# Kernel optimization log

Hardware: AMD Instinct MI355X
Metric: run time of the kernel (lower is better)

The kernel has to match this reference:

```python
import jax, jax.numpy as jnp
import numpy as np

IMC = 256
EPS = 1e-6
BN_EPS = 1e-5
GRID = (69.12, 79.36)      # (depth, width) in meters
OFF = (0.0, -39.68, 0.0)   # (xoff, yoff, zoff)
RES = 0.64
ZMIN, ZMAX = -3.0, 2.76
SCALES = [0.25, 0.125, 0.0625, 0.03125, 0.015625]


def make_corners():
    # replicates make_grid(): corner lattice in lidar coords, shape [nz, nx, ny, 3]
    nx = int(round(GRID[0] / RES)) + 1   # 109
    ny = int(round(GRID[1] / RES)) + 1   # 125
    nz = int(round((ZMAX - ZMIN) / RES)) + 1  # 10
    xc = RES * np.arange(nx) + OFF[0]
    yc = GRID[1] - RES * np.arange(ny) + OFF[1]
    zc = ZMAX - RES * np.arange(nz)
    xx, yy = np.meshgrid(xc, yc, indexing='ij')
    base = np.stack([xx, yy, np.full_like(xx, OFF[2])], axis=-1)  # [nx,ny,3]
    zoffs = np.stack([np.zeros(nz), np.zeros(nz), zc], axis=-1)   # [nz,3]
    corners = base[None] + zoffs[:, None, None, :]
    return jnp.asarray(corners, jnp.float32)


def grid_sample(img, grid):
    # img [B,C,H,W]; grid [B,P,N,2] xy in [-1,1]; bilinear, zero padding, align_corners=False
    B, C, H, W = img.shape
    x = (grid[..., 0] + 1.0) * (W * 0.5) - 0.5
    y = (grid[..., 1] + 1.0) * (H * 0.5) - 0.5
    x0f = jnp.floor(x); y0f = jnp.floor(y)
    wx = (x - x0f).reshape(B, 1, -1)
    wy = (y - y0f).reshape(B, 1, -1)
    x0 = x0f.astype(jnp.int32); y0 = y0f.astype(jnp.int32)
    flat = img.reshape(B, C, H * W)
    def g(xi, yi):
        ok = ((xi >= 0) & (xi < W) & (yi >= 0) & (yi < H)).reshape(B, 1, -1)
        idx = (jnp.clip(yi, 0, H - 1) * W + jnp.clip(xi, 0, W - 1)).reshape(B, 1, -1)
        return jnp.take_along_axis(flat, idx, axis=2) * ok
    v00 = g(x0, y0); v01 = g(x0 + 1, y0); v10 = g(x0, y0 + 1); v11 = g(x0 + 1, y0 + 1)
    out = (v00 * (1 - wx) + v01 * wx) * (1 - wy) + (v10 * (1 - wx) + v11 * wx) * wy
    return out.reshape(B, C, grid.shape[1], grid.shape[2])


def oft(feats, calib, corners, scale, w, b):
    B, C, Hf, Wf = feats.shape
    # perspective projection of grid corners into the image plane
    hom = jnp.einsum('bij,zdwj->bzdwi', calib[:, :, :3], corners) + calib[:, None, None, None, :, 3]
    xy = hom[..., :2] / hom[..., 2:3]                      # [B,nz,nx,ny,2]
    img_size = jnp.array([Wf, Hf], jnp.float32) / scale
    nc = jnp.clip(2.0 * xy / img_size - 1.0, -1.0, 1.0)
    mn = jnp.minimum(nc[:, :-1, :-1, :-1], nc[:, :-1, 1:, :-1])
    mx = jnp.maximum(nc[:, 1:, 1:, 1:], nc[:, 1:, :-1, 1:])
    bbox = jnp.concatenate([mn, mx], axis=-1)              # [B,Zc,Dc,Wc,4]
    _, Zc, Dc, Wc, _ = bbox.shape
    bbox = bbox.reshape(B, Zc, Dc * Wc, 4)
    area = ((bbox[..., 2] - bbox[..., 0]) * (bbox[..., 3] - bbox[..., 1])
            * (Hf * Wf * 0.25) + EPS)[:, None]             # [B,1,Zc,N]
    visible = (area > EPS).astype(feats.dtype)
    ii = jnp.cumsum(jnp.cumsum(feats, axis=-1), axis=-2)   # integral image
    tl = grid_sample(ii, jnp.stack([bbox[..., 0], bbox[..., 1]], -1))
    br = grid_sample(ii, jnp.stack([bbox[..., 2], bbox[..., 3]], -1))
    tr = grid_sample(ii, jnp.stack([bbox[..., 2], bbox[..., 1]], -1))
    bl = grid_sample(ii, jnp.stack([bbox[..., 0], bbox[..., 3]], -1))
    vox = (tl + br - tr - bl) / area * visible             # [B,C,Zc,N]
    vox = vox.transpose(0, 3, 1, 2).reshape(B * Dc * Wc, C * Zc)
    ortho = jax.nn.relu(vox @ w.T + b).reshape(B, Dc, Wc, -1)
    return ortho.transpose(0, 3, 2, 1)                     # [B,imc,Wc,Dc]


def attention(x, aw, ab):
    s = jax.nn.sigmoid(x.mean(axis=(2, 3)) @ aw.T + ab)
    return x * s[:, :, None, None]


def conv3x3(x, w, stride):
    return jax.lax.conv_general_dilated(x, w, (stride, stride), ((1, 1), (1, 1)),
                                        dimension_numbers=('NCHW', 'OIHW', 'NCHW'))


def bn(x, g, b, m, v):
    scale = g / jnp.sqrt(v + BN_EPS)
    return (x - m[None, :, None, None]) * scale[None, :, None, None] + b[None, :, None, None]


def make_calib(B):
    K = np.array([[560.0, 0.0, 640.0], [0.0, 560.0, 192.0], [0.0, 0.0, 1.0]])
    Rt = np.array([[0.0, -1.0, 0.0, 0.05],   # lidar(x fwd, y left, z up) -> cam(x right, y down, z fwd)
                   [0.0, 0.0, -1.0, -0.30],
                   [1.0, 0.0, 0.0, 0.27]])
    P = K @ Rt
    return jnp.asarray(np.tile(P[None], (B, 1, 1)), jnp.float32)


def setup_inputs() -> dict:
    key = jax.random.key(0)
    ks = jax.random.split(key, 16)
    B = 1
    shapes = [(B, IMC, 96, 320), (B, IMC, 48, 160), (B, IMC, 24, 80), (B, IMC, 12, 40), (B, IMC, 6, 20)]
    feats = [jax.random.normal(ks[i], s, jnp.float32) * 0.1 for i, s in enumerate(shapes)]
    HC = 9 * IMC  # height_channels = int((2.76-(-3))/0.64 * 256) = 2304
    inp = {
        'feats04': feats[0], 'feats08': feats[1], 'feats16': feats[2],
        'feats32': feats[3], 'feats64': feats[4],
        'calib': make_calib(B),
        'oft_w': jax.random.normal(ks[5], (5, IMC, HC), jnp.float32) * 0.02,
        'oft_b': jax.random.normal(ks[6], (5, IMC), jnp.float32) * 0.02,
        'att_w': jax.random.normal(ks[7], (IMC, IMC), jnp.float32) * 0.05,
        'att_b': jnp.zeros((IMC,), jnp.float32),
        'conv1_w': jax.random.normal(ks[8], (IMC, IMC * 5, 3, 3), jnp.float32) * 0.02,
        'bn1_g': 1.0 + 0.1 * jax.random.normal(ks[9], (IMC,), jnp.float32),
        'bn1_b': 0.05 * jax.random.normal(ks[10], (IMC,), jnp.float32),
        'bn1_m': 0.05 * jax.random.normal(ks[11], (IMC,), jnp.float32),
        'bn1_v': jax.random.uniform(ks[12], (IMC,), jnp.float32, 0.5, 1.5),
        'conv2_w': jax.random.normal(ks[13], (IMC, IMC, 3, 3), jnp.float32) * 0.02,
        'bn2_g': 1.0 + 0.1 * jax.random.normal(ks[14], (IMC,), jnp.float32),
        'bn2_b': jnp.zeros((IMC,), jnp.float32),
        'bn2_m': jnp.zeros((IMC,), jnp.float32),
        'bn2_v': jax.random.uniform(ks[15], (IMC,), jnp.float32, 0.5, 1.5),
    }
    return inp


def reference(feats04, feats08, feats16, feats32, feats64, calib,
              oft_w, oft_b, att_w, att_b,
              conv1_w, bn1_g, bn1_b, bn1_m, bn1_v,
              conv2_w, bn2_g, bn2_b, bn2_m, bn2_v):
    corners = make_corners()
    feats = [feats04, feats08, feats16, feats32, feats64]
    orthos = [attention(oft(f, calib, corners, s, oft_w[i], oft_b[i]), att_w, att_b)
              for i, (f, s) in enumerate(zip(feats, SCALES))]
    x = jnp.concatenate(orthos, axis=1)            # [B, 5*imc, 124, 108]
    x = jax.nn.relu(bn(conv3x3(x, conv1_w, 2), bn1_g, bn1_b, bn1_m, bn1_v))
    x = jax.nn.relu(bn(conv3x3(x, conv2_w, 1), bn2_g, bn2_b, bn2_m, bn2_v))
    return x                                       # [B, imc, 62, 54]
```

## Files before the change

kernel.cpp:

```cpp
#include <hip/hip_runtime.h>

typedef __attribute__((ext_vector_type(8))) short short8;
typedef __attribute__((ext_vector_type(4))) float float4v;
typedef __attribute__((ext_vector_type(4))) int int4v;
typedef __attribute__((ext_vector_type(4))) unsigned short ushort4v;

#define NBOX 13392
#define ZC 9
#define KOFT 2304
#define NPIX 3348
#define NBLK0 105
#define NBLKC 27
#define TILEK 4096
#define NBSTRIDE 294912
#define OFT_SPLIT 4

__device__ __forceinline__ unsigned short f2bf(float f) {
  union { float f; unsigned int i; } v; v.f = f;
  unsigned int r = v.i + 0x7FFFu + ((v.i >> 16) & 1u);
  return (unsigned short)(r >> 16);
}
__device__ __forceinline__ float bf2f(unsigned short u) {
  union { unsigned int i; float f; } v; v.i = ((unsigned int)u) << 16; return v.f;
}
__device__ __forceinline__ float i2f(int i) {
  union { int i; float f; } v; v.i = i; return v.f;
}

__device__ __forceinline__ const int* uniform_ptr(const int* p) {
  unsigned lo = (unsigned)(uintptr_t)p;
  unsigned hi = (unsigned)((uintptr_t)p >> 32);
  lo = (unsigned)__builtin_amdgcn_readfirstlane((int)lo);
  hi = (unsigned)__builtin_amdgcn_readfirstlane((int)hi);
  return (const int*)(((uintptr_t)hi << 32) | (uintptr_t)lo);
}

__device__ __forceinline__ void async16(const unsigned short* g, unsigned short* l) {
  __builtin_amdgcn_global_load_lds(
      (const __attribute__((address_space(1))) unsigned int*)g,
      (__attribute__((address_space(3))) unsigned int*)l, 16, 0, 0);
}

__global__ void k_alpha_beta(const float* __restrict__ oft_b,
                             const float* __restrict__ g1, const float* __restrict__ b1,
                             const float* __restrict__ m1, const float* __restrict__ v1,
                             const float* __restrict__ g2, const float* __restrict__ b2,
                             const float* __restrict__ m2, const float* __restrict__ v2,
                             float* __restrict__ ALPHA, float* __restrict__ BETA,
                             float* __restrict__ MEANS, unsigned short* __restrict__ ZPAGE) {
  int g = blockIdx.x, c = threadIdx.x;
  float al, be;
  if (g < 5) { al = 1.f; be = oft_b[g * 256 + c]; MEANS[g * 256 + c] = 0.f; }
  else {
    const float* gg = (g == 5) ? g1 : g2;
    const float* bb = (g == 5) ? b1 : b2;
    const float* mm = (g == 5) ? m1 : m2;
    const float* vv = (g == 5) ? v1 : v2;
    al = gg[c] / sqrtf(vv[c] + 1e-5f);
    be = bb[c] - mm[c] * al;
  }
  ALPHA[g * 256 + c] = al; BETA[g * 256 + c] = be;
  if (g == 0) ZPAGE[c] = 0;
}

__global__ void k_wpermT(const float* __restrict__ w, unsigned short* __restrict__ wp) {
  int idx = blockIdx.x * 256 + threadIdx.x;
  int sc = idx / 589824;
  int r  = idx % 589824;
  int j   = r & 7;
  int row = (r >> 3) & 127;
  int kc  = (r >> 10) & 3;
  int cs  = r >> 12;
  int cb  = cs / 72, s = cs % 72;
  int oc = cb * 128 + row;
  int k  = s * 32 + kc * 8 + j;
  int z = k >> 8, c = k & 255;
  wp[idx] = f2bf(w[((size_t)sc * 256 + oc) * 2304 + c * 9 + z]);
}

__global__ void k_wperm1T(const float* __restrict__ w, const float* __restrict__ satt,
                          unsigned short* __restrict__ wp) {
  int idx = blockIdx.x * 256 + threadIdx.x;
  int j   = idx & 7;
  int row = (idx >> 3) & 127;
  int kc  = (idx >> 10) & 3;
  int rest = idx >> 12;
  int s = rest % 40; rest /= 40;
  int r = rest % 9;  int cb = rest / 9;
  int oc = cb * 128 + row;
  int ic = s * 32 + kc * 8 + j;
  wp[idx] = f2bf(w[(size_t)oc * 11520 + ic * 9 + r] * satt[ic]);
}

__global__ void k_wperm2T(const float* __restrict__ w, unsigned short* __restrict__ wp) {
  int idx = blockIdx.x * 256 + threadIdx.x;
  int j   = idx & 7;
  int row = (idx >> 3) & 127;
  int kc  = (idx >> 10) & 3;
  int rest = idx >> 12;
  int s = rest % 8; rest /= 8;
  int r = rest % 9; int cb = rest / 9;
  int oc = cb * 128 + row;
  int ic = s * 32 + kc * 8 + j;
  wp[idx] = f2bf(w[(size_t)oc * 2304 + ic * 9 + r]);
}

__global__ void k_taps(const float* __restrict__ calib, int* __restrict__ taps,
                       int Hf, int Wf, float areaScale) {
  int idx = blockIdx.x * 256 + threadIdx.x;
  if (idx >= ZC * NBOX) return;
  int z = idx / NBOX, n = idx % NBOX;
  int d = n / 124, wj = n % 124;
  float P[12];
#pragma unroll
  for (int i = 0; i < 12; ++i) P[i] = calib[i];
  auto proj = [&](int k, int i, int j, float& nxo, float& nyo) {
    float X = 0.64f * (float)i;
    float Y = 39.68f - 0.64f * (float)j;
    float Z = 2.76f - 0.64f * (float)k;
    float hx = P[0] * X + P[1] * Y + P[2]  * Z + P[3];
    float hy = P[4] * X + P[5] * Y + P[6]  * Z + P[7];
    float hz = P[8] * X + P[9] * Y + P[10] * Z + P[11];
    float px = hx / hz, py = hy / hz;
    nxo = 2.f * px / 1280.f - 1.f; nxo = fminf(fmaxf(nxo, -1.f), 1.f);
    nyo = 2.f * py / 384.f  - 1.f; nyo = fminf(fmaxf(nyo, -1.f), 1.f);
  };
  float ax, ay, bx, by, cx, cy, dx, dy;
  proj(z,     d,     wj,     ax, ay);
  proj(z,     d + 1, wj,     bx, by);
  proj(z + 1, d + 1, wj + 1, cx, cy);
  proj(z + 1, d,     wj + 1, dx, dy);
  float x0 = fminf(ax, bx), y0 = fminf(ay, by);
  float x1 = fmaxf(cx, dx), y1 = fmaxf(cy, dy);
  float rawA = (x1 - x0) * (y1 - y0) * areaScale;
  int* ob = taps + (size_t)idx * 32;
  if (!(rawA > 0.f)) { ob[0] = 0; return; }
  float inv = 1.f / (rawA + 1e-6f);

  float u0 = (x0 + 1.f) * ((float)Wf * 0.5f) - 0.5f;
  float u1 = (x1 + 1.f) * ((float)Wf * 0.5f) - 0.5f;
  float fu0 = floorf(u0), fu1 = floorf(u1);
  int cx0 = (int)fu0, cx1 = (int)fu1;
  float wx0 = u0 - fu0, wx1 = u1 - fu1;
  int xs[4]; float xw[4];
  xs[0] = cx0; xs[1] = cx0 + 1; xs[2] = cx1; xs[3] = cx1 + 1;
  xw[0] = (1.f - wx0) * inv; xw[1] = wx0 * inv;
  xw[2] = -(1.f - wx1) * inv; xw[3] = -wx1 * inv;
  int dcx = cx1 - cx0;
  if (dcx == 0)      { xw[0] += xw[2]; xw[1] += xw[3]; xw[2] = 0.f; xw[3] = 0.f; }
  else if (dcx == 1) { xw[1] += xw[2]; xw[2] = xw[3]; xs[2] = xs[3]; xw[3] = 0.f; }
#pragma unroll
  for (int j = 0; j < 4; ++j) {
    if (xs[j] < 0 || xs[j] >= Wf) xw[j] = 0.f;
    xs[j] = min(max(xs[j], 0), Wf - 1);
  }
#define CSWX(a, b) { if (xw[a] == 0.f && xw[b] != 0.f) { \
    float tw = xw[a]; xw[a] = xw[b]; xw[b] = tw; \
    int ts = xs[a]; xs[a] = xs[b]; xs[b] = ts; } }
  CSWX(0, 1) CSWX(2, 3) CSWX(0, 2) CSWX(1, 3) CSWX(1, 2)
#undef CSWX
  int nx = (xw[0] != 0.f) + (xw[1] != 0.f) + (xw[2] != 0.f) + (xw[3] != 0.f);

  float v0 = (y0 + 1.f) * ((float)Hf * 0.5f) - 0.5f;
  float v1 = (y1 + 1.f) * ((float)Hf * 0.5f) - 0.5f;
  float fv0 = floorf(v0), fv1 = floorf(v1);
  int ry0 = (int)fv0, ry1 = (int)fv1;
  float wy0 = v0 - fv0, wy1 = v1 - fv1;
  int ys[4]; float yw[4];
  ys[0] = ry0; ys[1] = ry0 + 1; ys[2] = ry1; ys[3] = ry1 + 1;
  yw[0] = 1.f - wy0; yw[1] = wy0; yw[2] = -(1.f - wy1); yw[3] = -wy1;
  int dcy = ry1 - ry0;
  if (dcy == 0)      { yw[0] += yw[2]; yw[1] += yw[3]; yw[2] = 0.f; yw[3] = 0.f; }
  else if (dcy == 1) { yw[1] += yw[2]; yw[2] = yw[3]; ys[2] = ys[3]; yw[3] = 0.f; }
#pragma unroll
  for (int j = 0; j < 4; ++j) {
    if (ys[j] < 0 || ys[j] >= Hf) yw[j] = 0.f;
    ys[j] = min(max(ys[j], 0), Hf - 1);
  }
#define CSWY(a, b) { if (yw[a] == 0.f && yw[b] != 0.f) { \
    float tw = yw[a]; yw[a] = yw[b]; yw[b] = tw; \
    int ts = ys[a]; ys[a] = ys[b]; ys[b] = ts; } }
  CSWY(0, 1) CSWY(2, 3) CSWY(0, 2) CSWY(1, 3) CSWY(1, 2)
#undef CSWY
  int ny = (yw[0] != 0.f) + (yw[1] != 0.f) + (yw[2] != 0.f) + (yw[3] != 0.f);

  if (nx == 0 || ny == 0) { ob[0] = 0; return; }

  int off[16]; float w[16];
#pragma unroll
  for (int r = 0; r < 4; ++r)
#pragma unroll
    for (int c = 0; c < 4; ++c) {
      off[r * 4 + c] = (ys[r] * Wf + xs[c]) * 1024;
      w[r * 4 + c] = yw[r] * xw[c];
    }
  off[0] |= (nx << 25) | (ny << 28);
  int4v* obv = (int4v*)ob;
#pragma unroll
  for (int i = 0; i < 4; ++i)
    obv[i] = (int4v){off[4 * i], off[4 * i + 1], off[4 * i + 2], off[4 * i + 3]};
  float4v* wb = (float4v*)obv;
#pragma unroll
  for (int i = 0; i < 4; ++i)
    wb[4 + i] = (float4v){w[4 * i], w[4 * i + 1], w[4 * i + 2], w[4 * i + 3]};
}

__global__ void k_transpose_all(const float* __restrict__ f0, const float* __restrict__ f1,
                                const float* __restrict__ f2, const float* __restrict__ f3,
                                const float* __restrict__ f4, float* __restrict__ II) {
  int b = blockIdx.x;
  int sc, cx;
  if (b < 480)      { sc = 0; cx = b; }
  else if (b < 600) { sc = 1; cx = b - 480; }
  else if (b < 630) { sc = 2; cx = b - 600; }
  else if (b < 638) { sc = 3; cx = b - 630; }
  else              { sc = 4; cx = b - 638; }
  const int Ss[5] = {30720, 7680, 1920, 480, 120};
  const size_t IIof[5] = {0, 7864320, 9830400, 10321920, 10444800};
  const float* srcs[5] = {f0, f1, f2, f3, f4};
  int S = Ss[sc];
  const float* src = srcs[sc];
  float* dst = II + IIof[sc];
  __shared__ float tile[64][65];
  int t = threadIdx.x;
  int wave = t >> 6, lane = t & 63;
  int s0 = cx * 64, c0 = blockIdx.y * 64;
#pragma unroll
  for (int i = 0; i < 16; ++i) {
    int c_l = wave * 16 + i;
    if (s0 + lane < S) tile[c_l][lane] = src[(size_t)(c0 + c_l) * S + s0 + lane];
  }
  __syncthreads();
#pragma unroll
  for (int i = 0; i < 16; ++i) {
    int s_l = wave * 16 + i;
    if (s0 + s_l < S) dst[(size_t)(s0 + s_l) * 256 + c0 + lane] = tile[lane][s_l];
  }
}

__global__ void k_cumw_all(float* __restrict__ II) {
  int b = blockIdx.x;
  int sc, h;
  if (b < 96)       { sc = 0; h = b; }
  else if (b < 144) { sc = 1; h = b - 96; }
  else if (b < 168) { sc = 2; h = b - 144; }
  else if (b < 180) { sc = 3; h = b - 168; }
  else              { sc = 4; h = b - 180; }
  const int Wfs[5] = {320, 160, 80, 40, 20};
  const size_t IIof[5] = {0, 7864320, 9830400, 10321920, 10444800};
  int Wf = Wfs[sc];
  float* p = II + IIof[sc] + (size_t)h * Wf * 256 + threadIdx.x;
  float acc = 0.f;
#pragma unroll 4
  for (int w = 0; w < Wf; ++w) { acc += p[(size_t)w * 256]; p[(size_t)w * 256] = acc; }
}

__global__ void k_cumh_all(float* __restrict__ II) {
  int b = blockIdx.x;
  int sc, w;
  if (b < 320)      { sc = 0; w = b; }
  else if (b < 480) { sc = 1; w = b - 320; }
  else if (b < 560) { sc = 2; w = b - 480; }
  else if (b < 600) { sc = 3; w = b - 560; }
  else              { sc = 4; w = b - 600; }
  const int Wfs[5] = {320, 160, 80, 40, 20};
  const int Hfs[5] = {96, 48, 24, 12, 6};
  const size_t IIof[5] = {0, 7864320, 9830400, 10321920, 10444800};
  int Hf = Hfs[sc];
  size_t stride = (size_t)Wfs[sc] * 256;
  float* p = II + IIof[sc] + (size_t)w * 256 + threadIdx.x;
  float acc = 0.f;
#pragma unroll 4
  for (int h = 0; h < Hf; ++h) { acc += p[h * stride]; p[h * stride] = acc; }
}

__global__ __launch_bounds__(512) void k_sample(const float* __restrict__ ii,
                                                const int* __restrict__ taps,
                                                unsigned short* __restrict__ voxT) {
  __shared__ unsigned short st[3][8][66][4];
  int t = threadIdx.x;
  int wave = t >> 6, lane = t & 63;
  int n = blockIdx.x * 8 + wave;
  int zg = blockIdx.y * 3;
  const char* iib = (const char*)ii + (lane << 4);
#pragma unroll
  for (int dz = 0; dz < 3; ++dz) {
    int z = zg + dz;
    const int* tb = uniform_ptr(taps + (size_t)(z * NBOX + n) * 32);
    int o_[16];
#pragma unroll
    for (int i = 0; i < 16; ++i) o_[i] = tb[i];
    unsigned h = (unsigned)o_[0];
    int nx = (h >> 25) & 7;
    int ny = (h >> 28) & 7;
    o_[0] = (int)(h & 0x01FFFFFFu);
    ushort4v o;
    if (ny == 0) {
      o[0] = 0; o[1] = 0; o[2] = 0; o[3] = 0;
    } else {
      float w_[16];
#pragma unroll
      for (int i = 0; i < 16; ++i) w_[i] = i2f(tb[16 + i]);
      float4v a0 = {0.f, 0.f, 0.f, 0.f}, a1 = a0;
#define TAP(i, acc) { float4v t_ = *(const float4v*)(iib + (size_t)(unsigned)o_[i]); acc += t_ * w_[i]; }
      TAP(0, a0)
      if (nx > 1) TAP(1, a1)
      if (nx > 2) TAP(2, a0)
      if (nx > 3) TAP(3, a1)
      if (ny > 1) {
        TAP(4, a0)
        if (nx > 1) TAP(5, a1)
        if (nx > 2) TAP(6, a0)
        if (nx > 3) TAP(7, a1)
      }
      if (ny > 2) {
        TAP(8, a0)
        if (nx > 1) TAP(9, a1)
        if (nx > 2) TAP(10, a0)
        if (nx > 3) TAP(11, a1)
      }
      if (ny > 3) {
        TAP(12, a0)
        if (nx > 1) TAP(13, a1)
        if (nx > 2) TAP(14, a0)
        if (nx > 3) TAP(15, a1)
      }
#undef TAP
      float4v acc = a0 + a1;
#pragma unroll
      for (int j = 0; j < 4; ++j) o[j] = f2bf(acc[j]);
    }
    *(ushort4v*)&st[dz][wave][lane][0] = o;
  }
  __syncthreads();
  int nb = (blockIdx.x * 8) >> 7;
  int r0 = (blockIdx.x * 8) & 127;
  unsigned short* outb = voxT + (size_t)nb * NBSTRIDE + (size_t)r0 * 32;
  int lane32 = t & 31;
  int row = lane32 >> 2, kc = lane32 & 3;
#pragma unroll
  for (int p = 0; p < 2; ++p) {
    int q = p * 16 + (t >> 5);
    if (q < 24) {
      int zq = q >> 3;
      int si = q & 7;
      short8 v = *(const short8*)&st[zq][row][si * 8 + kc * 2][0];
      *(short8*)(outb + (size_t)(zg + zq) * 32768 + (size_t)si * 4096
                 + (size_t)(row * 32 + kc * 8)) = v;
    }
  }
}

__global__ __launch_bounds__(256) void k_gemmT(
    const unsigned short* __restrict__ AT, const unsigned short* __restrict__ BT,
    float* __restrict__ part) {
  __shared__ unsigned short lsA[4096];
  __shared__ unsigned short lsB[4096];
  int t = threadIdx.x;
  int lane = t & 63, wave = t >> 6;
  int l15 = lane & 15, quad = lane >> 4;
  int nb = blockIdx.x, cb = blockIdx.y, ks = blockIdx.z;
  int wrow = (wave >> 1) * 64, wcol = (wave & 1) * 64;

  const unsigned short* ga = AT + (size_t)nb * NBSTRIDE + (size_t)ks * 18 * TILEK + t * 8;
  const unsigned short* gb = BT + (size_t)cb * NBSTRIDE + (size_t)ks * 18 * TILEK + t * 8;
  unsigned short* ldA = lsA + t * 8;
  unsigned short* ldB = lsB + t * 8;

  float4v acc[4][4];
#pragma unroll
  for (int mi = 0; mi < 4; ++mi)
#pragma unroll
    for (int ni = 0; ni < 4; ++ni) acc[mi][ni] = (float4v){0.f, 0.f, 0.f, 0.f};

  for (int s = 0; s < 18; ++s) {
    async16(ga, ldA);
    async16(ga + 2048, ldA + 2048);
    async16(gb, ldB);
    async16(gb + 2048, ldB + 2048);
    ga += TILEK; gb += TILEK;
    __syncthreads();
    short8 af[4], bf[4];
    const short8* pA = (const short8*)lsA;
    const short8* pB = (const short8*)lsB;
#pragma unroll
    for (int mi = 0; mi < 4; ++mi) af[mi] = pA[(wrow + mi * 16 + l15) * 4 + quad];
#pragma unroll
    for (int ni = 0; ni < 4; ++ni) bf[ni] = pB[quad * 128 + wcol + ni * 16 + l15];
#pragma unroll
    for (int mi = 0; mi < 4; ++mi)
#pragma unroll
      for (int ni = 0; ni < 4; ++ni)
        acc[mi][ni] = __builtin_amdgcn_mfma_f32_16x16x32_bf16(af[mi], bf[ni], acc[mi][ni], 0, 0, 0);
    __syncthreads();
  }

#pragma unroll
  for (int mi = 0; mi < 4; ++mi) {
    int nb0 = nb * 128 + wrow + mi * 16 + quad * 4;
#pragma unroll
    for (int j = 0; j < 4; ++j) {
      int nn = nb0 + j;
      if (nn < NBOX) {
#pragma unroll
        for (int ni = 0; ni < 4; ++ni) {
          int oc = cb * 128 + wcol + ni * 16 + l15;
          part[((size_t)ks * NBOX + nn) * 256 + oc] = acc[mi][ni][j];
        }
      }
    }
  }
}

__global__ void k_redoft(const float* __restrict__ part, const float* __restrict__ beta,
                         unsigned short* __restrict__ xbuf, int choff) {
  int n = blockIdx.x, oc = threadIdx.x;
  float v = part[(size_t)n * 256 + oc]
          + part[((size_t)NBOX + n) * 256 + oc]
          + part[((size_t)2 * NBOX + n) * 256 + oc]
          + part[((size_t)3 * NBOX + n) * 256 + oc];
  v += beta[oc];
  v = v > 0.f ? v : 0.f;
  xbuf[(size_t)n * 1280 + choff + oc] = f2bf(v);
}

template <int MODE>
__global__ __launch_bounds__(256) void k_gemmS(
    const unsigned short* __restrict__ A, const unsigned short* __restrict__ BT,
    float* __restrict__ part, const unsigned short* __restrict__ zpage) {
  constexpr int KIC   = (MODE == 1) ? 1280 : 256;
  constexpr int STEPS = KIC / 32;
  __shared__ unsigned short lsA[4096];
  __shared__ unsigned short lsB[4096];
  int t = threadIdx.x;
  int lane = t & 63, wave = t >> 6;
  int l15 = lane & 15, quad = lane >> 4;
  int n0 = blockIdx.x * 128, oc0 = blockIdx.y * 128;
  int r = blockIdx.z;
  int wrow = (wave >> 1) * 64, wcol = (wave & 1) * 64;
  int srow = t & 127, skc = t >> 7;

  int p = n0 + srow;
  int oy = p / 54, ox = p - oy * 54;
  int ky = r / 3, kx = r - ky * 3;
  bool valid; int sp;
  if (MODE == 1) {
    int ih = 2 * oy + ky - 1, iw = 2 * ox + kx - 1;
    valid = (p < NPIX) && ((unsigned)ih < 124u) && ((unsigned)iw < 108u);
    sp = iw * 124 + ih;
  } else {
    int ih = oy + ky - 1, iw = ox + kx - 1;
    valid = (p < NPIX) && ((unsigned)ih < 62u) && ((unsigned)iw < 54u);
    sp = ih * 54 + iw;
  }
  const unsigned short* ga = valid ? (A + (size_t)sp * KIC + skc * 8) : zpage;
  int astep = valid ? 32 : 0;
  const unsigned short* gb = BT + ((size_t)(blockIdx.y * 9 + r) * STEPS) * TILEK + t * 8;
  unsigned short* ldA = lsA + t * 8;
  unsigned short* ldB = lsB + t * 8;

  float4v acc[4][4];
#pragma unroll
  for (int mi = 0; mi < 4; ++mi)
#pragma unroll
    for (int ni = 0; ni < 4; ++ni) acc[mi][ni] = (float4v){0.f, 0.f, 0.f, 0.f};

  for (int s = 0; s < STEPS; ++s) {
    async16(ga, ldA);
    async16(ga + 16, ldA + 2048);
    async16(gb, ldB);
    async16(gb + 2048, ldB + 2048);
    ga += astep; gb += TILEK;
    __syncthreads();
    short8 af[4], bf[4];
    const short8* pA = (const short8*)lsA;
    const short8* pB = (const short8*)lsB;
#pragma unroll
    for (int mi = 0; mi < 4; ++mi) af[mi] = pA[quad * 128 + wrow + mi * 16 + l15];
#pragma unroll
    for (int ni = 0; ni < 4; ++ni) bf[ni] = pB[quad * 128 + wcol + ni * 16 + l15];
#pragma unroll
    for (int mi = 0; mi < 4; ++mi)
#pragma unroll
      for (int ni = 0; ni < 4; ++ni)
        acc[mi][ni] = __builtin_amdgcn_mfma_f32_16x16x32_bf16(af[mi], bf[ni], acc[mi][ni], 0, 0, 0);
    __syncthreads();
  }

#pragma unroll
  for (int mi = 0; mi < 4; ++mi) {
    int nb0 = n0 + wrow + mi * 16 + quad * 4;
#pragma unroll
    for (int j = 0; j < 4; ++j) {
      int nn = nb0 + j;
      if (nn < NPIX) {
#pragma unroll
        for (int ni = 0; ni < 4; ++ni) {
          int oc = oc0 + wcol + ni * 16 + l15;
          part[((size_t)r * NPIX + nn) * 256 + oc] = acc[mi][ni][j];
        }
      }
    }
  }
}

template <bool F32OUT>
__global__ void k_redconv(const float* __restrict__ part, const float* __restrict__ alpha,
                          const float* __restrict__ beta, void* __restrict__ outv) {
  int p = blockIdx.x, oc = threadIdx.x;
  float v = 0.f;
#pragma unroll
  for (int r = 0; r < 9; ++r) v += part[((size_t)r * NPIX + p) * 256 + oc];
  v = v * alpha[oc] + beta[oc];
  v = v > 0.f ? v : 0.f;
  if (F32OUT) ((float*)outv)[(size_t)oc * NPIX + p] = v;
  else ((unsigned short*)outv)[(size_t)p * 256 + oc] = f2bf(v);
}

__global__ void k_means2(const unsigned short* __restrict__ x, float* __restrict__ means) {
  int tid = threadIdx.x;
  int r0 = blockIdx.x * 64;
  float part[5] = {0.f, 0.f, 0.f, 0.f, 0.f};
  for (int i = 0; i < 64; ++i) {
    int row = r0 + i;
    if (row < NBOX) {
      const unsigned short* rp = x + (size_t)row * 1280;
#pragma unroll
      for (int g = 0; g < 5; ++g) part[g] += bf2f(rp[g * 256 + tid]);
    }
  }
#pragma unroll
  for (int g = 0; g < 5; ++g) atomicAdd(&means[g * 256 + tid], part[g]);
}

__global__ void k_att(const float* __restrict__ means, const float* __restrict__ aw,
                      const float* __restrict__ ab, float* __restrict__ satt) {
  int sc = blockIdx.x, c = threadIdx.x;
  __shared__ float m[256];
  m[c] = means[sc * 256 + c] * (1.f / (float)NBOX);
  __syncthreads();
  float acc = ab[c];
  for (int j = 0; j < 256; ++j) acc += m[j] * aw[c * 256 + j];
  satt[sc * 256 + c] = 1.f / (1.f + expf(-acc));
}

extern "C" void kernel_launch(void* const* d_in, const int* in_sizes, int n_in,
                              void* d_out, int out_size, void* d_ws, size_t ws_size,
                              hipStream_t stream) {
  const float* feats[5];
  for (int i = 0; i < 5; ++i) feats[i] = (const float*)d_in[i];
  const float* calib   = (const float*)d_in[5];
  const float* oft_w   = (const float*)d_in[6];
  const float* oft_b   = (const float*)d_in[7];
  const float* att_w   = (const float*)d_in[8];
  const float* att_b   = (const float*)d_in[9];
  const float* conv1_w = (const float*)d_in[10];
  const float* bn1g = (const float*)d_in[11];
  const float* bn1b = (const float*)d_in[12];
  const float* bn1m = (const float*)d_in[13];
  const float* bn1v = (const float*)d_in[14];
  const float* conv2_w = (const float*)d_in[15];
  const float* bn2g = (const float*)d_in[16];
  const float* bn2b = (const float*)d_in[17];
  const float* bn2m = (const float*)d_in[18];
  const float* bn2v = (const float*)d_in[19];

  char* ws = (char*)d_ws;
  size_t off = 0;
  auto alloc = [&](size_t bytes) -> void* {
    void* p = ws + off; off += (bytes + 255) & ~(size_t)255; return p;
  };
  unsigned short* WPERMT = (unsigned short*)alloc((size_t)5 * 589824 * 2);
  unsigned short* WC1T   = (unsigned short*)alloc((size_t)2949120 * 2);
  unsigned short* WC2T   = (unsigned short*)alloc((size_t)589824 * 2);
  float*          II     = (float*)alloc((size_t)10475520 * 4);
  unsigned short* VOXT   = (unsigned short*)alloc((size_t)NBLK0 * NBSTRIDE * 2);
  unsigned short* XBUF   = (unsigned short*)alloc((size_t)NBOX * 1280 * 2);
  unsigned short* Y1     = (unsigned short*)alloc((size_t)NPIX * 256 * 2);
  float*          PART   = (float*)alloc((size_t)OFT_SPLIT * NBOX * 256 * 4);
  float*          MEANS  = (float*)alloc(1280 * 4);
  float*          SATT   = (float*)alloc(1280 * 4);
  float*          ALPHA  = (float*)alloc(7 * 256 * 4);
  float*          BETA   = (float*)alloc(7 * 256 * 4);
  unsigned short* ZPAGE  = (unsigned short*)alloc(256 * 2);
  int* TAPS = (int*)PART;
  (void)ws_size; (void)in_sizes; (void)n_in; (void)out_size;

  static const int HFs[5] = {96, 48, 24, 12, 6};
  static const int WFs[5] = {320, 160, 80, 40, 20};
  static const size_t IIoff[5] = {0, 7864320, 9830400, 10321920, 10444800};

  k_alpha_beta<<<7, 256, 0, stream>>>(oft_b, bn1g, bn1b, bn1m, bn1v,
                                      bn2g, bn2b, bn2m, bn2v, ALPHA, BETA, MEANS, ZPAGE);
  k_wpermT<<<11520, 256, 0, stream>>>(oft_w, WPERMT);
  k_wperm2T<<<2304, 256, 0, stream>>>(conv2_w, WC2T);

  k_transpose_all<<<dim3(640, 4), 256, 0, stream>>>(feats[0], feats[1], feats[2],
                                                    feats[3], feats[4], II);
  k_cumw_all<<<186, 256, 0, stream>>>(II);
  k_cumh_all<<<620, 256, 0, stream>>>(II);

  for (int s = 0; s < 5; ++s) {
    k_taps<<<(ZC * NBOX + 255) / 256, 256, 0, stream>>>(
        calib, TAPS, HFs[s], WFs[s], (float)(HFs[s] * WFs[s]) * 0.25f);
    k_sample<<<dim3(NBOX / 8, 3), 512, 0, stream>>>(II + IIoff[s], TAPS, VOXT);
    k_gemmT<<<dim3(NBLK0, 2, OFT_SPLIT), 256, 0, stream>>>(
        VOXT, WPERMT + (size_t)s * 589824, PART);
    k_redoft<<<NBOX, 256, 0, stream>>>(PART, BETA + s * 256, XBUF, s * 256);
  }
  k_means2<<<(NBOX + 63) / 64, 256, 0, stream>>>(XBUF, MEANS);
  k_att<<<5, 256, 0, stream>>>(MEANS, att_w, att_b, SATT);
  k_wperm1T<<<11520, 256, 0, stream>>>(conv1_w, SATT, WC1T);

  k_gemmS<1><<<dim3(NBLKC, 2, 9), 256, 0, stream>>>(XBUF, WC1T, PART, ZPAGE);
  k_redconv<false><<<NPIX, 256, 0, stream>>>(PART, ALPHA + 5 * 256, BETA + 5 * 256, Y1);

  k_gemmS<2><<<dim3(NBLKC, 2, 9), 256, 0, stream>>>(Y1, WC2T, PART, ZPAGE);
  k_redconv<true><<<NPIX, 256, 0, stream>>>(PART, ALPHA + 6 * 256, BETA + 6 * 256, d_out);
}
```

Baseline: 897.2 us.

## Batch OFT GEMMs across scales with fused bias-ReLU epilogue, dropping split-K

```diff
diff --git a/kernel.cpp b/kernel.cpp
--- a/kernel.cpp
+++ b/kernel.cpp
@@ -13,7 +13,7 @@
 #define NBLKC 27
 #define TILEK 4096
 #define NBSTRIDE 294912
-#define OFT_SPLIT 4
+#define VOXSZ 30965760
 
 __device__ __forceinline__ unsigned short f2bf(float f) {
   union { float f; unsigned int i; } v; v.f = f;
@@ -351,6 +351,86 @@
   }
 }
 
+__global__ __launch_bounds__(256) void k_gemmT_all(
+    const unsigned short* __restrict__ AT, const unsigned short* __restrict__ BT,
+    const float* __restrict__ beta, unsigned short* __restrict__ xbuf, int s0) {
+  __shared__ unsigned short ls[8704];
+  unsigned short* lsA = ls;
+  unsigned short* lsB = ls + 4096;
+  int t = threadIdx.x;
+  int lane = t & 63, wave = t >> 6;
+  int l15 = lane & 15, quad = lane >> 4;
+  int nb = blockIdx.x, cb = blockIdx.y;
+  int slab = blockIdx.z, sc = s0 + slab;
+  int wrow = (wave >> 1) * 64, wcol = (wave & 1) * 64;
+
+  const unsigned short* ga = AT + (size_t)slab * VOXSZ + (size_t)nb * NBSTRIDE + t * 8;
+  const unsigned short* gb = BT + (size_t)sc * 589824 + (size_t)cb * NBSTRIDE + t * 8;
+  unsigned short* ldA = lsA + t * 8;
+  unsigned short* ldB = lsB + t * 8;
+
+  float4v acc[4][4];
+#pragma unroll
+  for (int mi = 0; mi < 4; ++mi)
+#pragma unroll
+    for (int ni = 0; ni < 4; ++ni) acc[mi][ni] = (float4v){0.f, 0.f, 0.f, 0.f};
+
+  for (int s = 0; s < 72; ++s) {
+    async16(ga, ldA);
+    async16(ga + 2048, ldA + 2048);
+    async16(gb, ldB);
+    async16(gb + 2048, ldB + 2048);
+    ga += TILEK; gb += TILEK;
+    __syncthreads();
+    short8 af[4], bf[4];
+    const short8* pA = (const short8*)lsA;
+    const short8* pB = (const short8*)lsB;
+#pragma unroll
+    for (int mi = 0; mi < 4; ++mi) af[mi] = pA[(wrow + mi * 16 + l15) * 4 + quad];
+#pragma unroll
+    for (int ni = 0; ni < 4; ++ni) bf[ni] = pB[quad * 128 + wcol + ni * 16 + l15];
+#pragma unroll
+    for (int mi = 0; mi < 4; ++mi)
+#pragma unroll
+      for (int ni = 0; ni < 4; ++ni)
+        acc[mi][ni] = __builtin_amdgcn_mfma_f32_16x16x32_bf16(af[mi], bf[ni], acc[mi][ni], 0, 0, 0);
+    __syncthreads();
+  }
+
+  float bval[4];
+#pragma unroll
+  for (int ni = 0; ni < 4; ++ni)
+    bval[ni] = beta[sc * 256 + cb * 128 + wcol + ni * 16 + l15];
+#pragma unroll
+  for (int ph = 0; ph < 2; ++ph) {
+    if (wrow == ph * 64) {
+#pragma unroll
+      for (int mi = 0; mi < 4; ++mi)
+#pragma unroll
+        for (int ni = 0; ni < 4; ++ni)
+#pragma unroll
+          for (int j = 0; j < 4; ++j) {
+            int row = mi * 16 + quad * 4 + j;
+            int col = wcol + ni * 16 + l15;
+            float v = acc[mi][ni][j] + bval[ni];
+            ls[row * 136 + col] = f2bf(v > 0.f ? v : 0.f);
+          }
+    }
+    __syncthreads();
+#pragma unroll
+    for (int it = 0; it < 4; ++it) {
+      int idx = it * 256 + t;
+      int row = idx >> 4, ch = idx & 15;
+      int nn = nb * 128 + ph * 64 + row;
+      if (nn < NBOX) {
+        short8 v = *(const short8*)&ls[row * 136 + ch * 8];
+        *(short8*)(xbuf + (size_t)nn * 1280 + sc * 256 + cb * 128 + ch * 8) = v;
+      }
+    }
+    __syncthreads();
+  }
+}
+
 __global__ __launch_bounds__(256) void k_gemmT(
     const unsigned short* __restrict__ AT, const unsigned short* __restrict__ BT,
     float* __restrict__ part) {
@@ -574,17 +654,38 @@
   unsigned short* WC1T   = (unsigned short*)alloc((size_t)2949120 * 2);
   unsigned short* WC2T   = (unsigned short*)alloc((size_t)589824 * 2);
   float*          II     = (float*)alloc((size_t)10475520 * 4);
-  unsigned short* VOXT   = (unsigned short*)alloc((size_t)NBLK0 * NBSTRIDE * 2);
   unsigned short* XBUF   = (unsigned short*)alloc((size_t)NBOX * 1280 * 2);
   unsigned short* Y1     = (unsigned short*)alloc((size_t)NPIX * 256 * 2);
-  float*          PART   = (float*)alloc((size_t)OFT_SPLIT * NBOX * 256 * 4);
   float*          MEANS  = (float*)alloc(1280 * 4);
   float*          SATT   = (float*)alloc(1280 * 4);
   float*          ALPHA  = (float*)alloc(7 * 256 * 4);
   float*          BETA   = (float*)alloc(7 * 256 * 4);
   unsigned short* ZPAGE  = (unsigned short*)alloc(256 * 2);
-  int* TAPS = (int*)PART;
-  (void)ws_size; (void)in_sizes; (void)n_in; (void)out_size;
+
+  const size_t SLAB   = (size_t)VOXSZ * 2;
+  const size_t TAPSZ  = (size_t)ZC * NBOX * 128;
+  const size_t PARTSZ = (size_t)4 * NBOX * 256 * 4;
+  size_t rem = (ws_size > off) ? ws_size - off : 0;
+
+  int NS;
+  int* TAPS; unsigned short* VOXT; float* PART;
+  if (rem >= 5 * SLAB) {
+    NS = 5;
+    VOXT = (unsigned short*)alloc(5 * SLAB);
+    TAPS = (int*)XBUF;
+    PART = (float*)VOXT;
+  } else if (rem >= 2 * SLAB + TAPSZ) {
+    NS = (int)((rem - TAPSZ) / SLAB); if (NS > 4) NS = 4;
+    TAPS = (int*)alloc(TAPSZ);
+    VOXT = (unsigned short*)alloc((size_t)NS * SLAB);
+    PART = (float*)VOXT;
+  } else {
+    NS = 0;
+    VOXT = (unsigned short*)alloc(SLAB);
+    PART = (float*)alloc(PARTSZ);
+    TAPS = (int*)PART;
+  }
+  (void)in_sizes; (void)n_in; (void)out_size;
 
   static const int HFs[5] = {96, 48, 24, 12, 6};
   static const int WFs[5] = {320, 160, 80, 40, 20};
@@ -600,14 +701,30 @@
   k_cumw_all<<<186, 256, 0, stream>>>(II);
   k_cumh_all<<<620, 256, 0, stream>>>(II);
 
-  for (int s = 0; s < 5; ++s) {
-    k_taps<<<(ZC * NBOX + 255) / 256, 256, 0, stream>>>(
-        calib, TAPS, HFs[s], WFs[s], (float)(HFs[s] * WFs[s]) * 0.25f);
-    k_sample<<<dim3(NBOX / 8, 3), 512, 0, stream>>>(II + IIoff[s], TAPS, VOXT);
-    k_gemmT<<<dim3(NBLK0, 2, OFT_SPLIT), 256, 0, stream>>>(
-        VOXT, WPERMT + (size_t)s * 589824, PART);
-    k_redoft<<<NBOX, 256, 0, stream>>>(PART, BETA + s * 256, XBUF, s * 256);
-  }
+  if (NS > 0) {
+    int g0 = 0;
+    while (g0 < 5) {
+      int gsz = 5 - g0; if (gsz > NS) gsz = NS;
+      for (int s = g0; s < g0 + gsz; ++s) {
+        k_taps<<<(ZC * NBOX + 255) / 256, 256, 0, stream>>>(
+            calib, TAPS, HFs[s], WFs[s], (float)(HFs[s] * WFs[s]) * 0.25f);
+        k_sample<<<dim3(NBOX / 8, 3), 512, 0, stream>>>(
+            II + IIoff[s], TAPS, VOXT + (size_t)(s - g0) * VOXSZ);
+      }
+      k_gemmT_all<<<dim3(NBLK0, 2, gsz), 256, 0, stream>>>(VOXT, WPERMT, BETA, XBUF, g0);
+      g0 += gsz;
+    }
+  } else {
+    for (int s = 0; s < 5; ++s) {
+      k_taps<<<(ZC * NBOX + 255) / 256, 256, 0, stream>>>(
+          calib, TAPS, HFs[s], WFs[s], (float)(HFs[s] * WFs[s]) * 0.25f);
+      k_sample<<<dim3(NBOX / 8, 3), 512, 0, stream>>>(II + IIoff[s], TAPS, VOXT);
+      k_gemmT<<<dim3(NBLK0, 2, 4), 256, 0, stream>>>(
+          VOXT, WPERMT + (size_t)s * 589824, PART);
+      k_redoft<<<NBOX, 256, 0, stream>>>(PART, BETA + s * 256, XBUF, s * 256);
+    }
+  }
+
   k_means2<<<(NBOX + 63) / 64, 256, 0, stream>>>(XBUF, MEANS);
   k_att<<<5, 256, 0, stream>>>(MEANS, att_w, att_b, SATT);
   k_wperm1T<<<11520, 256, 0, stream>>>(conv1_w, SATT, WC1T);
```

Result: faster. 847.6 us (-5.5%).
